# Performance work log

Hardware: AMD Instinct MI355X
Metric: run time of the kernel (lower is better)

Reference implementation:

```python
import jax, jax.numpy as jnp
import numpy as np
from math import sqrt

N = 4096      # points
I = 64        # in_channels
H = 64        # hidden_units
O = 64        # out_channels
CUTS = 8
GROUPS = 4
RADIUS = 1.0
BLK = 128     # i-block size for the pairwise interaction (KeOps-style tiling)
EPS = 1e-5


def leaky(x):
    return jnp.where(x >= 0, x, 0.2 * x)


def group_norm(x, w, b):
    # x: (N, C). Matches torch GroupNorm on input (1, C, N):
    # stats per group over (C//GROUPS, N) jointly, affine per channel.
    n, c = x.shape
    xg = x.reshape(n, GROUPS, c // GROUPS)
    mean = xg.mean(axis=(0, 2), keepdims=True)
    var = ((xg - mean) ** 2).mean(axis=(0, 2), keepdims=True)
    xn = ((xg - mean) * jax.lax.rsqrt(var + EPS)).reshape(n, c)
    return xn * w + b


def setup_inputs() -> dict:
    key = jax.random.key(0)
    ks = jax.random.split(key, 16)
    rn = lambda k, s, sc=1.0: jax.random.normal(k, s, jnp.float32) * sc
    # conv MLP init as in the torch module
    A1 = rn(ks[3], (CUTS, 3))                                   # nn.init.normal_
    c1 = jax.random.uniform(ks[4], (CUTS,)) * 0.8 * jnp.sqrt((A1 ** 2).sum(-1))
    A2 = jax.random.uniform(ks[5], (H, CUTS), minval=-1.0 / np.sqrt(CUTS), maxval=1.0 / np.sqrt(CUTS))
    c2 = rn(ks[6], (H,)) * 0.5 * jnp.sqrt((A2 ** 2).sum(-1))
    return {
        "points": rn(ks[0], (N, 3)),
        "nuv": rn(ks[1], (N, 3, 3)),
        "features": rn(ks[2], (N, I)),
        "W_in1": rn(ks[7], (H, I), 1.0 / np.sqrt(I)), "b_in1": jnp.zeros((H,)),
        "W_in2": rn(ks[8], (H, H), 1.0 / np.sqrt(H)), "b_in2": jnp.zeros((H,)),
        "gn_in_w": jnp.ones((H,)), "gn_in_b": jnp.zeros((H,)),
        "A1": A1, "c1": c1, "A2": A2, "c2": c2,
        "W_out1": rn(ks[9], (O, H), 1.0 / np.sqrt(H)), "b_out1": jnp.zeros((O,)),
        "W_out2": rn(ks[10], (O, O), 1.0 / np.sqrt(O)), "b_out2": jnp.zeros((O,)),
        "gn_out_w": jnp.ones((O,)), "gn_out_b": jnp.zeros((O,)),
    }


def reference(points, nuv, features, W_in1, b_in1, W_in2, b_in2, gn_in_w, gn_in_b,
              A1, c1, A2, c2, W_out1, b_out1, W_out2, b_out2, gn_out_w, gn_out_b):
    # 1. net_in MLP + GroupNorm over (1, H, N)
    f = leaky(leaky(features @ W_in1.T + b_in1) @ W_in2.T + b_in2)
    f = group_norm(f, gn_in_w, gn_in_b)                      # (N, H)

    pts = points / (sqrt(2.0) * RADIUS)                      # scaled coords
    n_j = jax.lax.stop_gradient(nuv[:, 0, :])                # j-side normals are detached

    # 2. pairwise quasi-geodesic interaction, tiled over i-blocks.
    # Per-head loop in the original just slices rows of A2/c2 and channels of f;
    # computing the full H-dim conv and reducing is the identical math.
    @jax.checkpoint
    def block(args):
        xi, nuvi = args                                      # (BLK,3), (BLK,3,3)
        diff = pts[None, :, :] - xi[:, None, :]              # (BLK, N, 3) = x_j - x_i
        dot = nuvi[:, 0, :] @ n_j.T                          # (BLK, N) <n_i, n_j>
        d2 = (diff ** 2).sum(-1) * (2.0 - dot) ** 2          # quasi-geodesic d^2
        w = jnp.exp(-d2)                                     # gaussian window w_ij
        X = jnp.einsum('bij,bnj->bni', nuvi, diff)           # P_ij in local basis (BLK,N,3)
        h = jax.nn.relu(jnp.einsum('bni,ci->bnc', X, A1) + c1)   # (BLK,N,CUTS)
        Xc = jax.nn.relu(jnp.einsum('bnc,hc->bnh', h, A2) + c2)  # (BLK,N,H)
        return jnp.einsum('bn,bnh,nh->bh', w, Xc, f)         # sum over j -> (BLK,H)

    out = jax.lax.map(block, (pts.reshape(-1, BLK, 3), nuv.reshape(-1, BLK, 3, 3)))
    out = out.reshape(N, H)

    # 3. net_out MLP + GroupNorm
    g = leaky(leaky(out @ W_out1.T + b_out1) @ W_out2.T + b_out2)
    return group_norm(g, gn_out_w, gn_out_b)                 # (N, O)
```

## Files before the change

### kernel.cpp

```cpp
#include <hip/hip_runtime.h>
#include <hip/hip_bf16.h>
#include <math.h>

#define N_PTS 4096
#define INV_SQRT2 0.70710678118654752440f

typedef float f32x4 __attribute__((ext_vector_type(4)));
typedef float f32x2 __attribute__((ext_vector_type(2)));
typedef short s16x4 __attribute__((ext_vector_type(4)));
typedef short s16x8 __attribute__((ext_vector_type(8)));
typedef _Float16 f16x2 __attribute__((ext_vector_type(2)));

__device__ inline short f2bf(float x) {
    __hip_bfloat16 h = __float2bfloat16(x);
    return __builtin_bit_cast(short, h);
}

__device__ inline unsigned pk_trunc(float hi, float lo) {
    return __builtin_amdgcn_perm(__builtin_bit_cast(unsigned, hi),
                                 __builtin_bit_cast(unsigned, lo),
                                 0x07060302u);
}
__device__ inline unsigned pk_relu(unsigned x) {
    f16x2 v = __builtin_bit_cast(f16x2, x);
    f16x2 z = {(_Float16)0.f, (_Float16)0.f};
    return __builtin_bit_cast(unsigned, __builtin_elementwise_max(v, z));
}
__device__ inline float rfl(float x) {
    return __builtin_bit_cast(float, __builtin_amdgcn_readfirstlane(__builtin_bit_cast(int, x)));
}
__device__ inline f32x2 bc2(float s) { return (f32x2){s, s}; }
__device__ inline f32x2 fma2(f32x2 a, f32x2 b, f32x2 c) {
    return __builtin_elementwise_fma(a, b, c);
}

#if defined(__has_builtin)
#  if __has_builtin(__builtin_amdgcn_mfma_f32_16x16x16bf16_1k)
#    define MFMA16(a, b, c) __builtin_amdgcn_mfma_f32_16x16x16bf16_1k((a), (b), (c), 0, 0, 0)
#    define HAVE_MFMA16 1
#  elif __has_builtin(__builtin_amdgcn_mfma_f32_16x16x16_bf16)
#    define MFMA16(a, b, c) __builtin_amdgcn_mfma_f32_16x16x16_bf16((a), (b), (c), 0, 0, 0)
#    define HAVE_MFMA16 1
#  endif
#endif
#ifndef HAVE_MFMA16
__device__ inline f32x4 mfma16_asm(s16x4 a, s16x4 b, f32x4 c) {
    asm volatile("s_nop 1\n\tv_mfma_f32_16x16x16_bf16 %0, %1, %2, %0"
                 : "+v"(c) : "v"(a), "v"(b));
    return c;
}
#  define MFMA16(a, b, c) mfma16_asm((a), (b), (c))
#endif

#define MFMA32(a, b, c) __builtin_amdgcn_mfma_f32_16x16x32_bf16((a), (b), (c), 0, 0, 0)

#if defined(__has_builtin) && __has_builtin(__builtin_amdgcn_global_load_lds)
#  define HAVE_GLDS 1
#endif

__global__ __launch_bounds__(256) void mlp_gn_kernel(
    const float* __restrict__ inp, int extra,
    const float* __restrict__ W1, const float* __restrict__ b1,
    const float* __restrict__ W2, const float* __restrict__ b2,
    float* __restrict__ pre_out, float* __restrict__ partials)
{
    __shared__ float in_s[4][64];
    __shared__ float h1_s[4][64];
    __shared__ float red_s[4][8];

    const int tid = threadIdx.x;
    const int lane = tid & 63;
    const int wid = tid >> 6;
    const int n0 = blockIdx.x * 4;

    float xin = inp[n0 * 64 + tid];
    for (int s = 1; s <= extra; ++s)
        xin += inp[(size_t)s * (N_PTS * 64) + n0 * 64 + tid];
    in_s[wid][lane] = xin;
    __syncthreads();

    const int c = lane;
    float h = b1[c];
#pragma unroll
    for (int k4 = 0; k4 < 16; ++k4) {
        float4 wv = *(const float4*)&W1[c * 64 + k4 * 4];
        h = fmaf(in_s[wid][k4*4+0], wv.x, h);
        h = fmaf(in_s[wid][k4*4+1], wv.y, h);
        h = fmaf(in_s[wid][k4*4+2], wv.z, h);
        h = fmaf(in_s[wid][k4*4+3], wv.w, h);
    }
    h = (h >= 0.f) ? h : 0.2f * h;
    h1_s[wid][c] = h;
    __syncthreads();

    float g = b2[c];
#pragma unroll
    for (int k4 = 0; k4 < 16; ++k4) {
        float4 wv = *(const float4*)&W2[c * 64 + k4 * 4];
        g = fmaf(h1_s[wid][k4*4+0], wv.x, g);
        g = fmaf(h1_s[wid][k4*4+1], wv.y, g);
        g = fmaf(h1_s[wid][k4*4+2], wv.z, g);
        g = fmaf(h1_s[wid][k4*4+3], wv.w, g);
    }
    g = (g >= 0.f) ? g : 0.2f * g;
    pre_out[n0 * 64 + tid] = g;

    float v = g, v2 = g * g;
#pragma unroll
    for (int m = 1; m < 16; m <<= 1) {
        v  += __shfl_xor(v,  m, 64);
        v2 += __shfl_xor(v2, m, 64);
    }
    if ((lane & 15) == 0) {
        int grp = lane >> 4;
        red_s[wid][grp * 2 + 0] = v;
        red_s[wid][grp * 2 + 1] = v2;
    }
    __syncthreads();
    if (tid < 8) {
        int grp = tid >> 1, which = tid & 1;
        float s = red_s[0][grp*2+which] + red_s[1][grp*2+which]
                + red_s[2][grp*2+which] + red_s[3][grp*2+which];
        partials[blockIdx.x * 8 + grp * 2 + which] = s;
    }
}

__global__ __launch_bounds__(256) void finalize_kernel(
    const float* __restrict__ partials, int nblocks,
    const float* __restrict__ gw, const float* __restrict__ gb,
    float* __restrict__ ss)
{
    __shared__ float red[8][32];
    __shared__ float mean_s[4], inv_s[4];
    const int t = threadIdx.x;
    const int s = t >> 5, slot = t & 31;
    float acc = 0.f;
    for (int b = slot; b < nblocks; b += 32) acc += partials[b * 8 + s];
    red[s][slot] = acc;
    __syncthreads();
    if (t < 8) {
        float v = 0.f;
#pragma unroll
        for (int k = 0; k < 32; ++k) v += red[t][k];
        red[t][0] = v;
    }
    __syncthreads();
    if (t < 4) {
        float S = red[t * 2][0], SS = red[t * 2 + 1][0];
        const float cnt = (float)N_PTS * 16.f;
        float mean = S / cnt;
        float var = SS / cnt - mean * mean;
        mean_s[t] = mean;
        inv_s[t] = rsqrtf(var + 1e-5f);
    }
    __syncthreads();
    if (t < 64) {
        int grp = t >> 4;
        float sc = gw[t] * inv_s[grp];
        ss[t] = sc;
        ss[64 + t] = gb[t] - mean_s[grp] * sc;
    }
}

__global__ __launch_bounds__(256) void fnt_kernel(
    const float* __restrict__ f_pre, const float* __restrict__ ss,
    short* __restrict__ fn_sw,
    const float* __restrict__ points, const float* __restrict__ nuv,
    float* __restrict__ ptn4)
{
    const int h = blockIdx.x >> 4;
    const int j = ((blockIdx.x & 15) << 8) + threadIdx.x;
    float v = f_pre[j * 64 + h] * ss[h] + ss[64 + h];
    const int t = j >> 6, jj = j & 63;
    const int jsub = jj >> 4, g = (jj >> 2) & 3, r = jj & 3;
    const int u = g * 4 + jsub, p = u >> 1, lo = u & 1;
    const int pp = p ^ (h & 7);
    fn_sw[t * 4096 + h * 64 + pp * 8 + lo * 4 + r] = f2bf(v);

    if (blockIdx.x < 16) {
        const int pt = blockIdx.x * 256 + threadIdx.x;
        float sx = points[pt*3+0] * INV_SQRT2;
        float sy = points[pt*3+1] * INV_SQRT2;
        float sz = points[pt*3+2] * INV_SQRT2;
        float nx = nuv[pt*9+0], ny = nuv[pt*9+1], nz = nuv[pt*9+2];
        *(float4*)&ptn4[pt*8 + 0] = (float4){sx, sy, sz, 0.f};
        *(float4*)&ptn4[pt*8 + 4] = (float4){nx, ny, nz, 0.f};
    }
}

__global__ __launch_bounds__(256, 4) void pairwise_kernel(
    const float* __restrict__ nuv,
    const float* __restrict__ ptn4,
    const short* __restrict__ fn_sw,
    const float* __restrict__ A1, const float* __restrict__ c1,
    const float* __restrict__ A2, const float* __restrict__ c2,
    float* __restrict__ out_part, int nt, int jshift)
{
    __shared__ __align__(16) short FS[4096];
    __shared__ __align__(16) short P_s[8][768];

    const int tid = threadIdx.x;
    const int l = tid & 63;
    const int wid = tid >> 6;
    const int g = l >> 4;
    const int hl = l & 15;

    const int js = blockIdx.x & ((1 << jshift) - 1);
    const int ig = blockIdx.x >> jshift;
    const int i0 = ig * 8 + wid * 2;
    const int tmask = nt - 1;

    f32x2 nv2[9];
#pragma unroll
    for (int k = 0; k < 9; ++k)
        nv2[k] = (f32x2){rfl(nuv[i0 * 9 + k]), rfl(nuv[(i0 + 1) * 9 + k])};
    const f32x2 pix2 = (f32x2){rfl(ptn4[i0*8+0]), rfl(ptn4[(i0+1)*8+0])};
    const f32x2 piy2 = (f32x2){rfl(ptn4[i0*8+1]), rfl(ptn4[(i0+1)*8+1])};
    const f32x2 piz2 = (f32x2){rfl(ptn4[i0*8+2]), rfl(ptn4[(i0+1)*8+2])};

    float a1v[8][3], c1v[8];
#pragma unroll
    for (int cc = 0; cc < 8; ++cc) {
        a1v[cc][0] = A1[cc*3+0]; a1v[cc][1] = A1[cc*3+1]; a1v[cc][2] = A1[cc*3+2];
        c1v[cc] = c1[cc];
    }

    s16x4 A2sB[4];
#pragma unroll
    for (int ht = 0; ht < 4; ++ht) {
        const int h = ht * 16 + hl;
        s16x4 v;
#pragma unroll
        for (int r = 0; r < 4; ++r) {
            const int cc = 4 * g + r;
            float val = (cc < 8) ? A2[h*8 + cc] : ((cc == 8) ? c2[h] : 0.f);
            v[r] = f2bf(val);
        }
        A2sB[ht] = v;
    }

    f32x4 acc0[4], acc1[4];
#pragma unroll
    for (int ht = 0; ht < 4; ++ht) {
        acc0[ht] = (f32x4){0.f, 0.f, 0.f, 0.f};
        acc1[ht] = (f32x4){0.f, 0.f, 0.f, 0.f};
    }
    const f32x4 Zzero = (f32x4){0.f, 0.f, 0.f, 0.f};

    const char* FSb = (const char*)&FS[0];
    const int fs_off0 = hl * 128 + ((((g << 1) | 0) ^ (hl & 7)) << 4);
    const int fs_off1 = hl * 128 + ((((g << 1) | 1) ^ (hl & 7)) << 4);

    auto stage = [&](int t) {
        const short* src = fn_sw + (size_t)(js * nt + t) * 4096;
#ifdef HAVE_GLDS
        const short* s0 = src + wid * 1024 + l * 8;
        short* d0 = &FS[wid * 1024];
        __builtin_amdgcn_global_load_lds((const unsigned int*)s0,
                                         (unsigned int*)d0, 16, 0, 0);
        __builtin_amdgcn_global_load_lds((const unsigned int*)(s0 + 512),
                                         (unsigned int*)(d0 + 512), 16, 0, 0);
#else
        s16x8 a = *(const s16x8*)(src + tid * 16);
        s16x8 b = *(const s16x8*)(src + tid * 16 + 8);
        *(s16x8*)&FS[tid * 16] = a;
        *(s16x8*)&FS[tid * 16 + 8] = b;
#endif
    };

    const float* pbase = ptn4 + (size_t)(js * nt) * 64 * 8;
    float4 pj_c = *(const float4*)&pbase[l * 8];
    float4 nj_c = *(const float4*)&pbase[l * 8 + 4];
    stage(0);

    for (int t = 0; t < nt; ++t) {
        __syncthreads();

        s16x8 Fr0[4], Fr1[4];
#pragma unroll
        for (int ht = 0; ht < 4; ++ht) {
            Fr0[ht] = *(const s16x8*)(FSb + ht * 2048 + fs_off0);
            Fr1[ht] = *(const s16x8*)(FSb + ht * 2048 + fs_off1);
        }
        __syncthreads();
        if (t < nt - 1) stage(t + 1);

        const int tn = (t + 1) & tmask;
        float4 pj_n = *(const float4*)&pbase[(tn * 64 + l) * 8];
        float4 nj_n = *(const float4*)&pbase[(tn * 64 + l) * 8 + 4];

        {
            f32x2 dx = bc2(pj_c.x) - pix2;
            f32x2 dy = bc2(pj_c.y) - piy2;
            f32x2 dz = bc2(pj_c.z) - piz2;
            f32x2 s1 = fma2(dz, dz, fma2(dy, dy, dx * dx));
            f32x2 dt = fma2(nv2[2], bc2(nj_c.z),
                       fma2(nv2[1], bc2(nj_c.y), nv2[0] * bc2(nj_c.x)));
            f32x2 t2 = bc2(2.f) - dt;
            f32x2 d2 = (s1 * t2) * t2;
            float w0 = __expf(-d2[0]);
            float w1 = __expf(-d2[1]);
            f32x2 wp = (f32x2){w0, w1};
            f32x2 X0 = fma2(nv2[2], dz, fma2(nv2[1], dy, nv2[0] * dx));
            f32x2 X1 = fma2(nv2[5], dz, fma2(nv2[4], dy, nv2[3] * dx));
            f32x2 X2 = fma2(nv2[8], dz, fma2(nv2[7], dy, nv2[6] * dx));

            f32x2 hv[8];
#pragma unroll
            for (int cc = 0; cc < 8; ++cc) {
                f32x2 tt = fma2(bc2(a1v[cc][2]), X2,
                           fma2(bc2(a1v[cc][1]), X1,
                           fma2(bc2(a1v[cc][0]), X0, bc2(c1v[cc]))));
                hv[cc] = tt * wp;
            }
            {
                int2 ra, rb, rc;
                ra.x = (int)pk_relu(pk_trunc(hv[1][0], hv[0][0]));
                ra.y = (int)pk_relu(pk_trunc(hv[3][0], hv[2][0]));
                rb.x = (int)pk_relu(pk_trunc(hv[5][0], hv[4][0]));
                rb.y = (int)pk_relu(pk_trunc(hv[7][0], hv[6][0]));
                rc.x = (int)(__builtin_bit_cast(unsigned, w0) >> 16);
                rc.y = 0;
                short* rp = &P_s[wid * 2 + 0][l * 12];
                *(int2*)(rp + 0) = ra;
                *(int2*)(rp + 4) = rb;
                *(int2*)(rp + 8) = rc;
            }
            {
                int2 ra, rb, rc;
                ra.x = (int)pk_relu(pk_trunc(hv[1][1], hv[0][1]));
                ra.y = (int)pk_relu(pk_trunc(hv[3][1], hv[2][1]));
                rb.x = (int)pk_relu(pk_trunc(hv[5][1], hv[4][1]));
                rb.y = (int)pk_relu(pk_trunc(hv[7][1], hv[6][1]));
                rc.x = (int)(__builtin_bit_cast(unsigned, w1) >> 16);
                rc.y = 0;
                short* rp = &P_s[wid * 2 + 1][l * 12];
                *(int2*)(rp + 0) = ra;
                *(int2*)(rp + 4) = rb;
                *(int2*)(rp + 8) = rc;
            }
        }

#pragma unroll
        for (int jp = 0; jp < 2; ++jp) {
            const int j0 = (jp * 2 + 0) * 16 + hl;
            const int j1 = (jp * 2 + 1) * 16 + hl;
            const s16x4 Af00 = *(const s16x4*)&P_s[wid*2+0][j0 * 12 + 4 * g];
            const s16x4 Af01 = *(const s16x4*)&P_s[wid*2+0][j1 * 12 + 4 * g];
            const s16x4 Af10 = *(const s16x4*)&P_s[wid*2+1][j0 * 12 + 4 * g];
            const s16x4 Af11 = *(const s16x4*)&P_s[wid*2+1][j1 * 12 + 4 * g];
#pragma unroll
            for (int ht = 0; ht < 4; ++ht) {
                const s16x8 Fv = jp ? Fr1[ht] : Fr0[ht];
                f32x4 Za = MFMA16(Af00, A2sB[ht], Zzero);
                f32x4 Zb = MFMA16(Af01, A2sB[ht], Zzero);
                int4 b0;
                b0.x = (int)pk_relu(pk_trunc(Za[1], Za[0]));
                b0.y = (int)pk_relu(pk_trunc(Za[3], Za[2]));
                b0.z = (int)pk_relu(pk_trunc(Zb[1], Zb[0]));
                b0.w = (int)pk_relu(pk_trunc(Zb[3], Zb[2]));
                acc0[ht] = MFMA32(Fv, __builtin_bit_cast(s16x8, b0), acc0[ht]);
                f32x4 Zc = MFMA16(Af10, A2sB[ht], Zzero);
                f32x4 Zd = MFMA16(Af11, A2sB[ht], Zzero);
                int4 b1;
                b1.x = (int)pk_relu(pk_trunc(Zc[1], Zc[0]));
                b1.y = (int)pk_relu(pk_trunc(Zc[3], Zc[2]));
                b1.z = (int)pk_relu(pk_trunc(Zd[1], Zd[0]));
                b1.w = (int)pk_relu(pk_trunc(Zd[3], Zd[2]));
                acc1[ht] = MFMA32(Fv, __builtin_bit_cast(s16x8, b1), acc1[ht]);
            }
        }
        pj_c = pj_n; nj_c = nj_n;
    }

    asm volatile("s_nop 7\n\ts_nop 7" ::: );

    if (g == (hl >> 2)) {
        const int r = hl & 3;
        float* ob = out_part + (size_t)js * (N_PTS * 64);
#pragma unroll
        for (int ht = 0; ht < 4; ++ht) {
            float v0 = (r == 0) ? acc0[ht][0] : (r == 1) ? acc0[ht][1]
                     : (r == 2) ? acc0[ht][2] : acc0[ht][3];
            float v1 = (r == 0) ? acc1[ht][0] : (r == 1) ? acc1[ht][1]
                     : (r == 2) ? acc1[ht][2] : acc1[ht][3];
            ob[(i0 + 0) * 64 + ht * 16 + hl] = v0;
            ob[(i0 + 1) * 64 + ht * 16 + hl] = v1;
        }
    }
}

__global__ __launch_bounds__(256) void apply_kernel(
    const float* __restrict__ pre, const float* __restrict__ ss,
    float* __restrict__ out)
{
    int idx = blockIdx.x * 256 + threadIdx.x;
    int c = idx & 63;
    out[idx] = pre[idx] * ss[c] + ss[64 + c];
}

extern "C" void kernel_launch(void* const* d_in, const int* in_sizes, int n_in,
                              void* d_out, int out_size, void* d_ws, size_t ws_size,
                              hipStream_t stream) {
    const float* points   = (const float*)d_in[0];
    const float* nuv      = (const float*)d_in[1];
    const float* features = (const float*)d_in[2];
    const float* W_in1    = (const float*)d_in[3];
    const float* b_in1    = (const float*)d_in[4];
    const float* W_in2    = (const float*)d_in[5];
    const float* b_in2    = (const float*)d_in[6];
    const float* gn_in_w  = (const float*)d_in[7];
    const float* gn_in_b  = (const float*)d_in[8];
    const float* A1       = (const float*)d_in[9];
    const float* c1       = (const float*)d_in[10];
    const float* A2       = (const float*)d_in[11];
    const float* c2       = (const float*)d_in[12];
    const float* W_out1   = (const float*)d_in[13];
    const float* b_out1   = (const float*)d_in[14];
    const float* W_out2   = (const float*)d_in[15];
    const float* b_out2   = (const float*)d_in[16];
    const float* gn_out_w = (const float*)d_in[17];
    const float* gn_out_b = (const float*)d_in[18];

    const size_t MB = 1048576;
    const int JS = (ws_size >= 5 * MB) ? 4 : 2;
    const int jshift = (JS == 4) ? 2 : 1;
    const int nt = 64 / JS;
    const size_t op_bytes = (size_t)JS * N_PTS * 64 * 4;

    char* ws = (char*)d_ws;
    float* out_part = (float*)(ws + 0);
    float* f_pre    = (float*)(ws + 0);
    float* g_pre    = (float*)(ws + 0);
    short* fn_sw    = (short*)(ws + op_bytes);
    float* ptn4     = (float*)(ws + op_bytes + 524288);
    char*  tail     = ws + op_bytes + 524288 + 131072;
    float* part_in  = (float*)(tail);
    float* part_out = (float*)(tail + 32768);
    float* ss_in    = (float*)(tail + 65536);
    float* ss_out   = (float*)(tail + 66048);

    float* outp = (float*)d_out;

    mlp_gn_kernel<<<1024, 256, 0, stream>>>(features, 0, W_in1, b_in1,
                                            W_in2, b_in2, f_pre, part_in);
    finalize_kernel<<<1, 256, 0, stream>>>(part_in, 1024, gn_in_w, gn_in_b, ss_in);
    fnt_kernel<<<1024, 256, 0, stream>>>(f_pre, ss_in, fn_sw, points, nuv, ptn4);

    pairwise_kernel<<<512 * JS, 256, 0, stream>>>(nuv, ptn4, fn_sw,
                                                  A1, c1, A2, c2, out_part,
                                                  nt, jshift);

    mlp_gn_kernel<<<1024, 256, 0, stream>>>(out_part, JS - 1, W_out1, b_out1,
                                            W_out2, b_out2, g_pre, part_out);
    finalize_kernel<<<1, 256, 0, stream>>>(part_out, 1024, gn_out_w, gn_out_b, ss_out);

    apply_kernel<<<1024, 256, 0, stream>>>(g_pre, ss_out, outp);
}
```

Baseline: 172.2 us.

## Double-buffer tiles, compute MFMA A-fragments in registers, fold A1 into local basis

The pairwise kernel now double-buffers the feature tile and a new point/normal tile in LDS, which removes one __syncthreads per iteration. Each lane computes its own MFMA A-operand cut values directly in registers, so the P_s shared-memory round trip goes away. A1 is pre-multiplied by the local nuv basis once per block so each cut is a single 3-term FMA on diff. In exchange some pairwise geometry is recomputed redundantly across lane groups, LDS use doubles, and the occupancy hint of 4 waves per SIMD is dropped.

Result: slower. 208.4 us (+21.1%).

```diff
diff --git a/kernel.cpp b/kernel.cpp
--- a/kernel.cpp
+++ b/kernel.cpp
@@ -188,7 +188,7 @@
     }
 }
 
-__global__ __launch_bounds__(256, 4) void pairwise_kernel(
+__global__ __launch_bounds__(256) void pairwise_kernel(
     const float* __restrict__ nuv,
     const float* __restrict__ ptn4,
     const short* __restrict__ fn_sw,
@@ -196,8 +196,8 @@
     const float* __restrict__ A2, const float* __restrict__ c2,
     float* __restrict__ out_part, int nt, int jshift)
 {
-    __shared__ __align__(16) short FS[4096];
-    __shared__ __align__(16) short P_s[8][768];
+    __shared__ __align__(16) short FS[2][4096];
+    __shared__ __align__(16) float PT[2][512];
 
     const int tid = threadIdx.x;
     const int l = tid & 63;
@@ -208,7 +208,6 @@
     const int js = blockIdx.x & ((1 << jshift) - 1);
     const int ig = blockIdx.x >> jshift;
     const int i0 = ig * 8 + wid * 2;
-    const int tmask = nt - 1;
 
     f32x2 nv2[9];
 #pragma unroll
@@ -218,11 +217,23 @@
     const f32x2 piy2 = (f32x2){rfl(ptn4[i0*8+1]), rfl(ptn4[(i0+1)*8+1])};
     const f32x2 piz2 = (f32x2){rfl(ptn4[i0*8+2]), rfl(ptn4[(i0+1)*8+2])};
 
-    float a1v[8][3], c1v[8];
-#pragma unroll
-    for (int cc = 0; cc < 8; ++cc) {
-        a1v[cc][0] = A1[cc*3+0]; a1v[cc][1] = A1[cc*3+1]; a1v[cc][2] = A1[cc*3+2];
-        c1v[cc] = c1[cc];
+    f32x2 cm0[4], cm1[4], cm2[4], cb[4];
+#pragma unroll
+    for (int r = 0; r < 4; ++r) {
+        const int k = 4 * g + r;
+        if (k < 8) {
+            float a0 = A1[k*3+0], a1 = A1[k*3+1], a2 = A1[k*3+2];
+            cm0[r] = fma2(bc2(a2), nv2[6], fma2(bc2(a1), nv2[3], bc2(a0) * nv2[0]));
+            cm1[r] = fma2(bc2(a2), nv2[7], fma2(bc2(a1), nv2[4], bc2(a0) * nv2[1]));
+            cm2[r] = fma2(bc2(a2), nv2[8], fma2(bc2(a1), nv2[5], bc2(a0) * nv2[2]));
+            cb[r]  = bc2(c1[k]);
+        } else if (k == 8) {
+            cm0[r] = bc2(0.f); cm1[r] = bc2(0.f); cm2[r] = bc2(0.f);
+            cb[r]  = bc2(1.f);
+        } else {
+            cm0[r] = bc2(0.f); cm1[r] = bc2(0.f); cm2[r] = bc2(0.f);
+            cb[r]  = bc2(0.f);
+        }
     }
 
     s16x4 A2sB[4];
@@ -247,130 +258,101 @@
     }
     const f32x4 Zzero = (f32x4){0.f, 0.f, 0.f, 0.f};
 
-    const char* FSb = (const char*)&FS[0];
     const int fs_off0 = hl * 128 + ((((g << 1) | 0) ^ (hl & 7)) << 4);
     const int fs_off1 = hl * 128 + ((((g << 1) | 1) ^ (hl & 7)) << 4);
 
-    auto stage = [&](int t) {
-        const short* src = fn_sw + (size_t)(js * nt + t) * 4096;
+    auto stage = [&](int buf, int t) {
+        const short* src  = fn_sw + (size_t)(js * nt + t) * 4096;
+        const float* psrc = ptn4 + (size_t)(js * nt + t) * 512;
 #ifdef HAVE_GLDS
         const short* s0 = src + wid * 1024 + l * 8;
-        short* d0 = &FS[wid * 1024];
+        short* d0 = &FS[buf][wid * 1024];
         __builtin_amdgcn_global_load_lds((const unsigned int*)s0,
                                          (unsigned int*)d0, 16, 0, 0);
         __builtin_amdgcn_global_load_lds((const unsigned int*)(s0 + 512),
                                          (unsigned int*)(d0 + 512), 16, 0, 0);
+        if (wid < 2) {
+            const float* p0 = psrc + wid * 256 + l * 4;
+            float* q0 = &PT[buf][wid * 256];
+            __builtin_amdgcn_global_load_lds((const unsigned int*)p0,
+                                             (unsigned int*)q0, 16, 0, 0);
+        }
 #else
         s16x8 a = *(const s16x8*)(src + tid * 16);
         s16x8 b = *(const s16x8*)(src + tid * 16 + 8);
-        *(s16x8*)&FS[tid * 16] = a;
-        *(s16x8*)&FS[tid * 16 + 8] = b;
+        *(s16x8*)&FS[buf][tid * 16] = a;
+        *(s16x8*)&FS[buf][tid * 16 + 8] = b;
+        if (tid < 128) {
+            float4 pv = *(const float4*)(psrc + tid * 4);
+            *(float4*)&PT[buf][tid * 4] = pv;
+        }
 #endif
     };
 
-    const float* pbase = ptn4 + (size_t)(js * nt) * 64 * 8;
-    float4 pj_c = *(const float4*)&pbase[l * 8];
-    float4 nj_c = *(const float4*)&pbase[l * 8 + 4];
-    stage(0);
+    stage(0, 0);
 
     for (int t = 0; t < nt; ++t) {
+        const int cur = t & 1;
         __syncthreads();
-
-        s16x8 Fr0[4], Fr1[4];
-#pragma unroll
-        for (int ht = 0; ht < 4; ++ht) {
-            Fr0[ht] = *(const s16x8*)(FSb + ht * 2048 + fs_off0);
-            Fr1[ht] = *(const s16x8*)(FSb + ht * 2048 + fs_off1);
-        }
-        __syncthreads();
-        if (t < nt - 1) stage(t + 1);
-
-        const int tn = (t + 1) & tmask;
-        float4 pj_n = *(const float4*)&pbase[(tn * 64 + l) * 8];
-        float4 nj_n = *(const float4*)&pbase[(tn * 64 + l) * 8 + 4];
-
-        {
-            f32x2 dx = bc2(pj_c.x) - pix2;
-            f32x2 dy = bc2(pj_c.y) - piy2;
-            f32x2 dz = bc2(pj_c.z) - piz2;
-            f32x2 s1 = fma2(dz, dz, fma2(dy, dy, dx * dx));
-            f32x2 dt = fma2(nv2[2], bc2(nj_c.z),
-                       fma2(nv2[1], bc2(nj_c.y), nv2[0] * bc2(nj_c.x)));
-            f32x2 t2 = bc2(2.f) - dt;
-            f32x2 d2 = (s1 * t2) * t2;
-            float w0 = __expf(-d2[0]);
-            float w1 = __expf(-d2[1]);
-            f32x2 wp = (f32x2){w0, w1};
-            f32x2 X0 = fma2(nv2[2], dz, fma2(nv2[1], dy, nv2[0] * dx));
-            f32x2 X1 = fma2(nv2[5], dz, fma2(nv2[4], dy, nv2[3] * dx));
-            f32x2 X2 = fma2(nv2[8], dz, fma2(nv2[7], dy, nv2[6] * dx));
-
-            f32x2 hv[8];
-#pragma unroll
-            for (int cc = 0; cc < 8; ++cc) {
-                f32x2 tt = fma2(bc2(a1v[cc][2]), X2,
-                           fma2(bc2(a1v[cc][1]), X1,
-                           fma2(bc2(a1v[cc][0]), X0, bc2(c1v[cc]))));
-                hv[cc] = tt * wp;
+        if (t < nt - 1) stage(cur ^ 1, t + 1);
+        const char* FScur = (const char*)&FS[cur][0];
+
+#pragma unroll
+        for (int jp = 0; jp < 2; ++jp) {
+            s16x8 Fv[4];
+            const int fo = (jp == 0) ? fs_off0 : fs_off1;
+#pragma unroll
+            for (int ht = 0; ht < 4; ++ht)
+                Fv[ht] = *(const s16x8*)(FScur + ht * 2048 + fo);
+
+            s16x4 Afa[2], Afb[2];
+#pragma unroll
+            for (int lo = 0; lo < 2; ++lo) {
+                const int jr = (jp * 2 + lo) * 16 + hl;
+                float4 pj = *(const float4*)&PT[cur][jr * 8];
+                float4 nj = *(const float4*)&PT[cur][jr * 8 + 4];
+                f32x2 dx = bc2(pj.x) - pix2;
+                f32x2 dy = bc2(pj.y) - piy2;
+                f32x2 dz = bc2(pj.z) - piz2;
+                f32x2 s1 = fma2(dz, dz, fma2(dy, dy, dx * dx));
+                f32x2 dt = fma2(nv2[2], bc2(nj.z),
+                           fma2(nv2[1], bc2(nj.y), nv2[0] * bc2(nj.x)));
+                f32x2 t2 = bc2(2.f) - dt;
+                f32x2 d2 = (s1 * t2) * t2;
+                f32x2 wp = (f32x2){__expf(-d2[0]), __expf(-d2[1])};
+                f32x2 hv0 = fma2(cm2[0], dz, fma2(cm1[0], dy, fma2(cm0[0], dx, cb[0]))) * wp;
+                f32x2 hv1 = fma2(cm2[1], dz, fma2(cm1[1], dy, fma2(cm0[1], dx, cb[1]))) * wp;
+                f32x2 hv2 = fma2(cm2[2], dz, fma2(cm1[2], dy, fma2(cm0[2], dx, cb[2]))) * wp;
+                f32x2 hv3 = fma2(cm2[3], dz, fma2(cm1[3], dy, fma2(cm0[3], dx, cb[3]))) * wp;
+                int2 pa, pb;
+                pa.x = (int)pk_relu(pk_trunc(hv1[0], hv0[0]));
+                pa.y = (int)pk_relu(pk_trunc(hv3[0], hv2[0]));
+                pb.x = (int)pk_relu(pk_trunc(hv1[1], hv0[1]));
+                pb.y = (int)pk_relu(pk_trunc(hv3[1], hv2[1]));
+                Afa[lo] = __builtin_bit_cast(s16x4, pa);
+                Afb[lo] = __builtin_bit_cast(s16x4, pb);
             }
-            {
-                int2 ra, rb, rc;
-                ra.x = (int)pk_relu(pk_trunc(hv[1][0], hv[0][0]));
-                ra.y = (int)pk_relu(pk_trunc(hv[3][0], hv[2][0]));
-                rb.x = (int)pk_relu(pk_trunc(hv[5][0], hv[4][0]));
-                rb.y = (int)pk_relu(pk_trunc(hv[7][0], hv[6][0]));
-                rc.x = (int)(__builtin_bit_cast(unsigned, w0) >> 16);
-                rc.y = 0;
-                short* rp = &P_s[wid * 2 + 0][l * 12];
-                *(int2*)(rp + 0) = ra;
-                *(int2*)(rp + 4) = rb;
-                *(int2*)(rp + 8) = rc;
-            }
-            {
-                int2 ra, rb, rc;
-                ra.x = (int)pk_relu(pk_trunc(hv[1][1], hv[0][1]));
-                ra.y = (int)pk_relu(pk_trunc(hv[3][1], hv[2][1]));
-                rb.x = (int)pk_relu(pk_trunc(hv[5][1], hv[4][1]));
-                rb.y = (int)pk_relu(pk_trunc(hv[7][1], hv[6][1]));
-                rc.x = (int)(__builtin_bit_cast(unsigned, w1) >> 16);
-                rc.y = 0;
-                short* rp = &P_s[wid * 2 + 1][l * 12];
-                *(int2*)(rp + 0) = ra;
-                *(int2*)(rp + 4) = rb;
-                *(int2*)(rp + 8) = rc;
-            }
-        }
-
-#pragma unroll
-        for (int jp = 0; jp < 2; ++jp) {
-            const int j0 = (jp * 2 + 0) * 16 + hl;
-            const int j1 = (jp * 2 + 1) * 16 + hl;
-            const s16x4 Af00 = *(const s16x4*)&P_s[wid*2+0][j0 * 12 + 4 * g];
-            const s16x4 Af01 = *(const s16x4*)&P_s[wid*2+0][j1 * 12 + 4 * g];
-            const s16x4 Af10 = *(const s16x4*)&P_s[wid*2+1][j0 * 12 + 4 * g];
-            const s16x4 Af11 = *(const s16x4*)&P_s[wid*2+1][j1 * 12 + 4 * g];
+
 #pragma unroll
             for (int ht = 0; ht < 4; ++ht) {
-                const s16x8 Fv = jp ? Fr1[ht] : Fr0[ht];
-                f32x4 Za = MFMA16(Af00, A2sB[ht], Zzero);
-                f32x4 Zb = MFMA16(Af01, A2sB[ht], Zzero);
+                f32x4 Za = MFMA16(Afa[0], A2sB[ht], Zzero);
+                f32x4 Zb = MFMA16(Afa[1], A2sB[ht], Zzero);
                 int4 b0;
                 b0.x = (int)pk_relu(pk_trunc(Za[1], Za[0]));
                 b0.y = (int)pk_relu(pk_trunc(Za[3], Za[2]));
                 b0.z = (int)pk_relu(pk_trunc(Zb[1], Zb[0]));
                 b0.w = (int)pk_relu(pk_trunc(Zb[3], Zb[2]));
-                acc0[ht] = MFMA32(Fv, __builtin_bit_cast(s16x8, b0), acc0[ht]);
-                f32x4 Zc = MFMA16(Af10, A2sB[ht], Zzero);
-                f32x4 Zd = MFMA16(Af11, A2sB[ht], Zzero);
+                acc0[ht] = MFMA32(Fv[ht], __builtin_bit_cast(s16x8, b0), acc0[ht]);
+                f32x4 Zc = MFMA16(Afb[0], A2sB[ht], Zzero);
+                f32x4 Zd = MFMA16(Afb[1], A2sB[ht], Zzero);
                 int4 b1;
                 b1.x = (int)pk_relu(pk_trunc(Zc[1], Zc[0]));
                 b1.y = (int)pk_relu(pk_trunc(Zc[3], Zc[2]));
                 b1.z = (int)pk_relu(pk_trunc(Zd[1], Zd[0]));
                 b1.w = (int)pk_relu(pk_trunc(Zd[3], Zd[2]));
-                acc1[ht] = MFMA32(Fv, __builtin_bit_cast(s16x8, b1), acc1[ht]);
+                acc1[ht] = MFMA32(Fv[ht], __builtin_bit_cast(s16x8, b1), acc1[ht]);
             }
         }
-        pj_c = pj_n; nj_c = nj_n;
     }
 
     asm volatile("s_nop 7\n\ts_nop 7" ::: );
```

## Load feature tiles directly from global in MFMA fragment order, dropping LDS staging

Applied to the files above, without the earlier changes.

Relayouts the normalized feature buffer so each lane's MFMA B-fragment is a contiguous 16-byte chunk, and has each wave read its fragments straight from global/L2 instead of staging the tile through shared memory. This removes two block-wide barriers per j-tile and the LDS copy and reads, and frees LDS, which may allow more blocks per CU. In exchange every wave fetches the full feature tile itself, so global/L2 traffic per block rises fourfold, and the loads are no longer prefetched one tile ahead, which may expose latency.

Result: faster. 166.5 us, median of 2 (-3.3%).

```diff
diff --git a/kernel.cpp b/kernel.cpp
--- a/kernel.cpp
+++ b/kernel.cpp
@@ -54,10 +54,6 @@
 
 #define MFMA32(a, b, c) __builtin_amdgcn_mfma_f32_16x16x32_bf16((a), (b), (c), 0, 0, 0)
 
-#if defined(__has_builtin) && __has_builtin(__builtin_amdgcn_global_load_lds)
-#  define HAVE_GLDS 1
-#endif
-
 __global__ __launch_bounds__(256) void mlp_gn_kernel(
     const float* __restrict__ inp, int extra,
     const float* __restrict__ W1, const float* __restrict__ b1,
@@ -173,9 +169,10 @@
     float v = f_pre[j * 64 + h] * ss[h] + ss[64 + h];
     const int t = j >> 6, jj = j & 63;
     const int jsub = jj >> 4, g = (jj >> 2) & 3, r = jj & 3;
-    const int u = g * 4 + jsub, p = u >> 1, lo = u & 1;
-    const int pp = p ^ (h & 7);
-    fn_sw[t * 4096 + h * 64 + pp * 8 + lo * 4 + r] = f2bf(v);
+    const int jp = jsub >> 1, lo = jsub & 1;
+    const int ht = h >> 4, hl = h & 15;
+    const int unit = ((t * 2 + jp) * 4 + ht) * 64 + hl * 4 + g;
+    fn_sw[unit * 8 + lo * 4 + r] = f2bf(v);
 
     if (blockIdx.x < 16) {
         const int pt = blockIdx.x * 256 + threadIdx.x;
@@ -196,7 +193,6 @@
     const float* __restrict__ A2, const float* __restrict__ c2,
     float* __restrict__ out_part, int nt, int jshift)
 {
-    __shared__ __align__(16) short FS[4096];
     __shared__ __align__(16) short P_s[8][768];
 
     const int tid = threadIdx.x;
@@ -247,43 +243,21 @@
     }
     const f32x4 Zzero = (f32x4){0.f, 0.f, 0.f, 0.f};
 
-    const char* FSb = (const char*)&FS[0];
-    const int fs_off0 = hl * 128 + ((((g << 1) | 0) ^ (hl & 7)) << 4);
-    const int fs_off1 = hl * 128 + ((((g << 1) | 1) ^ (hl & 7)) << 4);
-
-    auto stage = [&](int t) {
-        const short* src = fn_sw + (size_t)(js * nt + t) * 4096;
-#ifdef HAVE_GLDS
-        const short* s0 = src + wid * 1024 + l * 8;
-        short* d0 = &FS[wid * 1024];
-        __builtin_amdgcn_global_load_lds((const unsigned int*)s0,
-                                         (unsigned int*)d0, 16, 0, 0);
-        __builtin_amdgcn_global_load_lds((const unsigned int*)(s0 + 512),
-                                         (unsigned int*)(d0 + 512), 16, 0, 0);
-#else
-        s16x8 a = *(const s16x8*)(src + tid * 16);
-        s16x8 b = *(const s16x8*)(src + tid * 16 + 8);
-        *(s16x8*)&FS[tid * 16] = a;
-        *(s16x8*)&FS[tid * 16 + 8] = b;
-#endif
-    };
-
-    const float* pbase = ptn4 + (size_t)(js * nt) * 64 * 8;
+    const int laneoff = (hl * 4 + g) * 8;
+    const short* fnb = fn_sw + (size_t)(js * nt) * 4096;
+    const float* pbase = ptn4 + (size_t)(js * nt) * 512;
+
     float4 pj_c = *(const float4*)&pbase[l * 8];
     float4 nj_c = *(const float4*)&pbase[l * 8 + 4];
-    stage(0);
 
     for (int t = 0; t < nt; ++t) {
-        __syncthreads();
-
-        s16x8 Fr0[4], Fr1[4];
-#pragma unroll
-        for (int ht = 0; ht < 4; ++ht) {
-            Fr0[ht] = *(const s16x8*)(FSb + ht * 2048 + fs_off0);
-            Fr1[ht] = *(const s16x8*)(FSb + ht * 2048 + fs_off1);
-        }
-        __syncthreads();
-        if (t < nt - 1) stage(t + 1);
+        const short* bt = fnb + t * 4096;
+        s16x8 Fv[2][4];
+#pragma unroll
+        for (int jp = 0; jp < 2; ++jp)
+#pragma unroll
+            for (int ht = 0; ht < 4; ++ht)
+                Fv[jp][ht] = *(const s16x8*)(bt + (jp * 4 + ht) * 512 + laneoff);
 
         const int tn = (t + 1) & tmask;
         float4 pj_n = *(const float4*)&pbase[(tn * 64 + l) * 8];
@@ -351,7 +325,7 @@
             const s16x4 Af11 = *(const s16x4*)&P_s[wid*2+1][j1 * 12 + 4 * g];
 #pragma unroll
             for (int ht = 0; ht < 4; ++ht) {
-                const s16x8 Fv = jp ? Fr1[ht] : Fr0[ht];
+                const s16x8 Fvv = Fv[jp][ht];
                 f32x4 Za = MFMA16(Af00, A2sB[ht], Zzero);
                 f32x4 Zb = MFMA16(Af01, A2sB[ht], Zzero);
                 int4 b0;
@@ -359,7 +333,7 @@
                 b0.y = (int)pk_relu(pk_trunc(Za[3], Za[2]));
                 b0.z = (int)pk_relu(pk_trunc(Zb[1], Zb[0]));
                 b0.w = (int)pk_relu(pk_trunc(Zb[3], Zb[2]));
-                acc0[ht] = MFMA32(Fv, __builtin_bit_cast(s16x8, b0), acc0[ht]);
+                acc0[ht] = MFMA32(Fvv, __builtin_bit_cast(s16x8, b0), acc0[ht]);
                 f32x4 Zc = MFMA16(Af10, A2sB[ht], Zzero);
                 f32x4 Zd = MFMA16(Af11, A2sB[ht], Zzero);
                 int4 b1;
@@ -367,7 +341,7 @@
                 b1.y = (int)pk_relu(pk_trunc(Zc[3], Zc[2]));
                 b1.z = (int)pk_relu(pk_trunc(Zd[1], Zd[0]));
                 b1.w = (int)pk_relu(pk_trunc(Zd[3], Zd[2]));
-                acc1[ht] = MFMA32(Fv, __builtin_bit_cast(s16x8, b1), acc1[ht]);
+                acc1[ht] = MFMA32(Fvv, __builtin_bit_cast(s16x8, b1), acc1[ht]);
             }
         }
         pj_c = pj_n; nj_c = nj_n;
```
